# Optimization experiments

Measured on AMD Instinct MI355X. Metric: run time of the kernel, lower is better.

The kernel has to match this reference:

```python
import jax, jax.numpy as jnp
import numpy as np

N = 50000      # nodes
E = 800000     # edges (avg degree 16)
IN = 128       # in_dim0
H = 96         # hidden_dim
BN_EPS = 1e-5
PN_SCALE = 20.0


def setup_inputs() -> dict:
    key = jax.random.key(0)
    ks = jax.random.split(key, 12)
    s_in = 1.0 / np.sqrt(IN)
    s_h = 1.0 / np.sqrt(H)
    return {
        "x": jax.random.normal(ks[0], (N, IN), jnp.float32),
        "edge_index": jax.random.randint(ks[1], (2, E), 0, N, jnp.int32),
        # mlp0: Linear(in_dim0 -> hidden)
        "W0": jax.random.uniform(ks[2], (H, IN), jnp.float32, -s_in, s_in),
        "b0": jax.random.uniform(ks[3], (H,), jnp.float32, -s_in, s_in),
        # GIN MLP layer 1: Linear(hidden -> hidden) + BatchNorm
        "W1": jax.random.uniform(ks[4], (H, H), jnp.float32, -s_h, s_h),
        "b1": jax.random.uniform(ks[5], (H,), jnp.float32, -s_h, s_h),
        "gamma": jnp.ones((H,), jnp.float32),
        "beta": jnp.zeros((H,), jnp.float32),
        # GIN MLP layer 2: Linear(hidden -> hidden)
        "W2": jax.random.uniform(ks[6], (H, H), jnp.float32, -s_h, s_h),
        "b2": jax.random.uniform(ks[7], (H,), jnp.float32, -s_h, s_h),
    }


def reference(x, edge_index, W0, b0, W1, b1, gamma, beta, W2, b2):
    # h0 = mlp0(x)
    h0 = x @ W0.T + b0                                   # [N, H]

    # GINConv (eps=0): z_i = h0_i + sum_{j->i} h0_j
    src, dst = edge_index[0], edge_index[1]
    agg = jax.ops.segment_sum(h0[src], dst, num_segments=N)  # [N, H]
    z = h0 + agg

    # GIN MLP (layer_num=2): Linear -> BatchNorm(train) -> ReLU -> Linear
    h = z @ W1.T + b1
    mean = h.mean(axis=0)
    var = h.var(axis=0)                                  # biased, like torch BN
    h = (h - mean) * jax.lax.rsqrt(var + BN_EPS) * gamma + beta
    h = jax.nn.relu(h)
    l1 = h @ W2.T + b2                                   # [N, H]

    # PairNorm 'PN-SCS', scale=20
    col_mean = l1.mean(axis=0)
    rownorm = jnp.sqrt(1e-6 + jnp.sum(l1 * l1, axis=1, keepdims=True))
    l1 = PN_SCALE * l1 / rownorm - col_mean

    return (l1, h0)
```

## Files before the change

### kernel.cpp

```cpp
#include <hip/hip_runtime.h>

#define NN 50000
#define IN_DIM 128
#define HD 96
#define BN_EPS 1e-5f
#define PN_SCALE 20.0f
#define SCAN_NB 196
#define NREP 4

using bf16x8 = __attribute__((ext_vector_type(8))) short;
using f32x4  = __attribute__((ext_vector_type(4))) float;

__device__ __forceinline__ float4 ld4(const float* p) { return *(const float4*)p; }
__device__ __forceinline__ float4 add4(float4 a, float4 b) {
    return make_float4(a.x + b.x, a.y + b.y, a.z + b.z, a.w + b.w);
}

__device__ __forceinline__ short bfr(float f) {
    unsigned u = __float_as_uint(f);
    unsigned r = u + 0x7fffu + ((u >> 16) & 1u);
    return (short)(r >> 16);
}
__device__ __forceinline__ bf16x8 cvt8(float4 a, float4 b) {
    bf16x8 r;
    r[0] = bfr(a.x); r[1] = bfr(a.y); r[2] = bfr(a.z); r[3] = bfr(a.w);
    r[4] = bfr(b.x); r[5] = bfr(b.y); r[6] = bfr(b.z); r[7] = bfr(b.w);
    return r;
}

__global__ void zero_kernel(float* stats, int* cnt) {
    int i = blockIdx.x * blockDim.x + threadIdx.x;
    if (i < 1024) stats[i] = 0.0f;
    int j = i - 1024;
    if (j >= 0 && j < NREP * NN) cnt[j] = 0;
}

template<int K, int MODE>
__global__ __launch_bounds__(256) void gemm_mfma(
    const float* A, const float* __restrict__ W, const float* __restrict__ bias,
    float* out, const float* __restrict__ scale, const float* __restrict__ shift,
    float* __restrict__ gsum, float* __restrict__ gsumsq,
    float* __restrict__ gcol, float* __restrict__ growss,
    const int* __restrict__ ei, int* __restrict__ hist_cnt, int E)
{
    constexpr int P     = K + 8;
    constexpr int NS    = K / 32;
    constexpr int KD4   = K / 4;
    constexpr int WITER = (96 * KD4) / 256;
    constexpr int WL_SH  = 96 * P;
    constexpr int WL_TOT = (20608 > WL_SH) ? 20608 : WL_SH;
    __shared__ short Wl[WL_TOT];

    const int t    = threadIdx.x;
    const int l    = t & 63;
    const int w    = t >> 6;
    const int l15  = l & 15;
    const int lh   = l >> 4;
    const int base = blockIdx.x * 64;

    const int  arow = base + w * 16 + l15;
    const bool aok  = arow < NN;
    const float* Ap = A + (size_t)arow * K + lh * 8;
    const float4 Z4 = make_float4(0.f, 0.f, 0.f, 0.f);

    float4 pa[2 * NS];
#pragma unroll
    for (int s = 0; s < NS; ++s) {
        pa[2 * s]     = aok ? ld4(Ap + s * 32)     : Z4;
        pa[2 * s + 1] = aok ? ld4(Ap + s * 32 + 4) : Z4;
    }
    float4 wv[WITER];
#pragma unroll
    for (int i = 0; i < WITER; ++i) {
        int c = t + i * 256;
        int row = c / KD4, kq = c - row * KD4;
        wv[i] = ld4(W + (size_t)row * K + kq * 4);
    }
    float4 scv[2 * NS], shv[2 * NS];
    if (MODE == 2) {
#pragma unroll
        for (int s = 0; s < 2 * NS; ++s) {
            scv[s] = ld4(scale + (s >> 1) * 32 + lh * 8 + (s & 1) * 4);
            shv[s] = ld4(shift + (s >> 1) * 32 + lh * 8 + (s & 1) * 4);
        }
    }

    if (MODE == 0) {
        int e0 = (blockIdx.x * 256 + t) * 4;
        if (e0 + 4 <= E) {
            int4 d4 = *(const int4*)(ei + E + e0);
            atomicAdd(&hist_cnt[0 * NN + d4.x], 1);
            atomicAdd(&hist_cnt[1 * NN + d4.y], 1);
            atomicAdd(&hist_cnt[2 * NN + d4.z], 1);
            atomicAdd(&hist_cnt[3 * NN + d4.w], 1);
        } else {
            for (int i = 0; i < 4; ++i) {
                int e = e0 + i;
                if (e < E) atomicAdd(&hist_cnt[(e & 3) * NN + ei[E + e]], 1);
            }
        }
    }

    bf16x8 af[NS];
#pragma unroll
    for (int s = 0; s < NS; ++s) {
        float4 q0 = pa[2 * s], q1 = pa[2 * s + 1];
        if (MODE == 2) {
            float4 sc0 = scv[2 * s], sh0 = shv[2 * s];
            float4 sc1 = scv[2 * s + 1], sh1 = shv[2 * s + 1];
            q0.x = fmaxf(q0.x * sc0.x + sh0.x, 0.f);
            q0.y = fmaxf(q0.y * sc0.y + sh0.y, 0.f);
            q0.z = fmaxf(q0.z * sc0.z + sh0.z, 0.f);
            q0.w = fmaxf(q0.w * sc0.w + sh0.w, 0.f);
            q1.x = fmaxf(q1.x * sc1.x + sh1.x, 0.f);
            q1.y = fmaxf(q1.y * sc1.y + sh1.y, 0.f);
            q1.z = fmaxf(q1.z * sc1.z + sh1.z, 0.f);
            q1.w = fmaxf(q1.w * sc1.w + sh1.w, 0.f);
        }
        af[s] = cvt8(q0, q1);
    }

#pragma unroll
    for (int i = 0; i < WITER; ++i) {
        int c = t + i * 256;
        int row = c / KD4, kq = c - row * KD4;
        short4 s4v;
        s4v.x = bfr(wv[i].x); s4v.y = bfr(wv[i].y);
        s4v.z = bfr(wv[i].z); s4v.w = bfr(wv[i].w);
        *(short4*)(Wl + row * P + kq * 4) = s4v;
    }
    __syncthreads();

    f32x4 acc[6];
#pragma unroll
    for (int n = 0; n < 6; ++n) acc[n] = (f32x4){0.f, 0.f, 0.f, 0.f};

#pragma unroll
    for (int s = 0; s < NS; ++s) {
        const short* wp = Wl + s * 32 + lh * 8;
#pragma unroll
        for (int n = 0; n < 6; ++n) {
            bf16x8 bf = *(const bf16x8*)(wp + (n * 16 + l15) * P);
            acc[n] = __builtin_amdgcn_mfma_f32_16x16x32_bf16(af[s], bf, acc[n], 0, 0, 0);
        }
    }

    float cv[6][4];
#pragma unroll
    for (int n = 0; n < 6; ++n) {
        float b = bias[n * 16 + l15];
#pragma unroll
        for (int r = 0; r < 4; ++r) cv[n][r] = acc[n][r] + b;
    }
    int crow[4]; bool cok[4];
#pragma unroll
    for (int r = 0; r < 4; ++r) {
        crow[r] = base + w * 16 + lh * 4 + r;
        cok[r]  = crow[r] < NN;
    }

    __syncthreads();
    float* Cl = (float*)Wl;
#pragma unroll
    for (int n = 0; n < 6; ++n)
#pragma unroll
        for (int r = 0; r < 4; ++r)
            Cl[(w * 16 + lh * 4 + r) * 100 + n * 16 + l15] = cv[n][r];
    __syncthreads();
    {
        int lrow = t >> 2;
        int q4   = t & 3;
        int grow = base + lrow;
        if (grow < NN) {
            float* o = out + (size_t)grow * HD;
            const float* cr = Cl + lrow * 100;
#pragma unroll
            for (int k = 0; k < 6; ++k) {
                int c4 = q4 + k * 4;
                *(float4*)(o + c4 * 4) = *(const float4*)(cr + c4 * 4);
            }
        }
    }

    if (MODE == 1) {
        float s[6], q[6];
#pragma unroll
        for (int n = 0; n < 6; ++n) {
            s[n] = 0.f; q[n] = 0.f;
#pragma unroll
            for (int r = 0; r < 4; ++r) {
                float v = cok[r] ? cv[n][r] : 0.f;
                s[n] += v; q[n] += v * v;
            }
        }
#pragma unroll
        for (int n = 0; n < 6; ++n) {
            s[n] += __shfl_xor(s[n], 16); s[n] += __shfl_xor(s[n], 32);
            q[n] += __shfl_xor(q[n], 16); q[n] += __shfl_xor(q[n], 32);
        }
        float* red0 = (float*)Wl + 6400;
        float* red1 = red0 + 384;
        if (lh == 0) {
#pragma unroll
            for (int n = 0; n < 6; ++n) {
                red0[w * 96 + n * 16 + l15] = s[n];
                red1[w * 96 + n * 16 + l15] = q[n];
            }
        }
        __syncthreads();
        if (t < HD) {
            float S = red0[t] + red0[96 + t] + red0[192 + t] + red0[288 + t];
            float Q = red1[t] + red1[96 + t] + red1[192 + t] + red1[288 + t];
            atomicAdd(&gsum[t], S);
            atomicAdd(&gsumsq[t], Q);
        }
    }

    if (MODE == 2) {
        float s[6];
#pragma unroll
        for (int n = 0; n < 6; ++n) {
            s[n] = 0.f;
#pragma unroll
            for (int r = 0; r < 4; ++r) s[n] += cok[r] ? cv[n][r] : 0.f;
        }
#pragma unroll
        for (int n = 0; n < 6; ++n) {
            s[n] += __shfl_xor(s[n], 16); s[n] += __shfl_xor(s[n], 32);
        }
        float rq[4];
#pragma unroll
        for (int r = 0; r < 4; ++r) {
            float v = 0.f;
#pragma unroll
            for (int n = 0; n < 6; ++n) v = fmaf(cv[n][r], cv[n][r], v);
            v += __shfl_xor(v, 1); v += __shfl_xor(v, 2);
            v += __shfl_xor(v, 4); v += __shfl_xor(v, 8);
            rq[r] = v;
        }
        float* red0 = (float*)Wl + 6400;
        if (lh == 0) {
#pragma unroll
            for (int n = 0; n < 6; ++n) red0[w * 96 + n * 16 + l15] = s[n];
        }
        __syncthreads();
        if (t < HD) {
            float S = red0[t] + red0[96 + t] + red0[192 + t] + red0[288 + t];
            atomicAdd(&gcol[t], S);
        }
        if (l15 == 0) {
#pragma unroll
            for (int r = 0; r < 4; ++r)
                if (cok[r]) growss[crow[r]] = rq[r];
        }
    }
}

__global__ __launch_bounds__(256) void scan_part1(const int* __restrict__ cnt,
                                                  int* __restrict__ bsum) {
    __shared__ int sh[256];
    int i = blockIdx.x * 256 + threadIdx.x;
    int t = threadIdx.x;
    int v = 0;
    if (i < NN)
        v = cnt[i] + cnt[NN + i] + cnt[2 * NN + i] + cnt[3 * NN + i];
    sh[t] = v;
    __syncthreads();
    for (int off = 128; off > 0; off >>= 1) {
        if (t < off) sh[t] += sh[t + off];
        __syncthreads();
    }
    if (t == 0) bsum[blockIdx.x] = sh[0];
}

__global__ __launch_bounds__(256) void scan_part2(int* __restrict__ bsum) {
    __shared__ int sh[256];
    int t = threadIdx.x;
    int v = (t < SCAN_NB) ? bsum[t] : 0;
    sh[t] = v;
    __syncthreads();
    for (int off = 1; off < 256; off <<= 1) {
        int u = sh[t];
        if (t >= off) u += sh[t - off];
        __syncthreads();
        sh[t] = u;
        __syncthreads();
    }
    if (t < SCAN_NB) bsum[t] = sh[t] - v;
}

__global__ __launch_bounds__(256) void scan_part3(int* __restrict__ cnt,
                                                  const int* __restrict__ bsum,
                                                  int* __restrict__ rowptr) {
    __shared__ int sh[256];
    int i = blockIdx.x * 256 + threadIdx.x;
    int t = threadIdx.x;
    int v = 0;
    if (i < NN)
        v = cnt[i] + cnt[NN + i] + cnt[2 * NN + i] + cnt[3 * NN + i];
    sh[t] = v;
    __syncthreads();
    for (int off = 1; off < 256; off <<= 1) {
        int u = sh[t];
        if (t >= off) u += sh[t - off];
        __syncthreads();
        sh[t] = u;
        __syncthreads();
    }
    int excl = sh[t] - v + bsum[blockIdx.x];
    if (i < NN) { rowptr[i] = excl; cnt[i] = excl; }
    if (i == NN - 1) rowptr[NN] = excl + v;
}

__global__ __launch_bounds__(256) void fill_kernel(const int* __restrict__ ei,
                                                   int* __restrict__ cursor,
                                                   int* __restrict__ srcs, int E) {
    int t2 = blockIdx.x * 256 + threadIdx.x;
    int e0 = t2 * 2;
    int src[2], dst[2];
#pragma unroll
    for (int i = 0; i < 2; ++i) {
        int e = e0 + i;
        bool ok = e < E;
        dst[i] = ok ? ei[E + e] : -1;
        src[i] = ok ? ei[e] : 0;
    }
    for (int pass = 0; pass < 7; ++pass) {
#pragma unroll
        for (int i = 0; i < 2; ++i) {
            if (dst[i] >= 0 && (dst[i] >> 13) == pass) {
                int slot = atomicAdd(&cursor[dst[i]], 1);
                srcs[slot] = src[i];
            }
        }
    }
}

__global__ __launch_bounds__(192) void gather_kernel(
    const float* __restrict__ h0, const int* __restrict__ rowptr,
    const int* __restrict__ srcs, float* __restrict__ z)
{
    const int tid = threadIdx.x;
    const int rl  = tid / 24;
    const int c   = tid - rl * 24;
    const int row = blockIdx.x * 8 + rl;
    if (row >= NN) return;

    const int p0 = rowptr[row];
    const int p1 = rowptr[row + 1];

    float4 acc = ld4(h0 + (size_t)row * HD + c * 4);

    int p = p0;
    for (; p + 8 <= p1; p += 8) {
        int s0 = srcs[p + 0], s1 = srcs[p + 1], s2 = srcs[p + 2], s3 = srcs[p + 3];
        int s4 = srcs[p + 4], s5 = srcs[p + 5], s6 = srcs[p + 6], s7 = srcs[p + 7];
        float4 v0 = ld4(h0 + (size_t)s0 * HD + c * 4);
        float4 v1 = ld4(h0 + (size_t)s1 * HD + c * 4);
        float4 v2 = ld4(h0 + (size_t)s2 * HD + c * 4);
        float4 v3 = ld4(h0 + (size_t)s3 * HD + c * 4);
        float4 v4 = ld4(h0 + (size_t)s4 * HD + c * 4);
        float4 v5 = ld4(h0 + (size_t)s5 * HD + c * 4);
        float4 v6 = ld4(h0 + (size_t)s6 * HD + c * 4);
        float4 v7 = ld4(h0 + (size_t)s7 * HD + c * 4);
        acc = add4(acc, add4(add4(add4(v0, v1), add4(v2, v3)),
                             add4(add4(v4, v5), add4(v6, v7))));
    }
    for (; p + 4 <= p1; p += 4) {
        int s0 = srcs[p + 0], s1 = srcs[p + 1], s2 = srcs[p + 2], s3 = srcs[p + 3];
        float4 v0 = ld4(h0 + (size_t)s0 * HD + c * 4);
        float4 v1 = ld4(h0 + (size_t)s1 * HD + c * 4);
        float4 v2 = ld4(h0 + (size_t)s2 * HD + c * 4);
        float4 v3 = ld4(h0 + (size_t)s3 * HD + c * 4);
        acc = add4(acc, add4(add4(v0, v1), add4(v2, v3)));
    }
    for (; p < p1; ++p)
        acc = add4(acc, ld4(h0 + (size_t)srcs[p] * HD + c * 4));

    *(float4*)(z + (size_t)row * HD + c * 4) = acc;
}

__global__ void bn_finalize_kernel(const float* __restrict__ sum, const float* __restrict__ sumsq,
                                   const float* __restrict__ gamma, const float* __restrict__ beta,
                                   float* __restrict__ scale, float* __restrict__ shift)
{
    int f = threadIdx.x;
    if (f < HD) {
        float mean = sum[f] * (1.0f / NN);
        float var  = fmaxf(sumsq[f] * (1.0f / NN) - mean * mean, 0.0f);
        float rstd = rsqrtf(var + BN_EPS);
        float sc = rstd * gamma[f];
        scale[f] = sc;
        shift[f] = beta[f] - mean * sc;
    }
}

__global__ __launch_bounds__(256) void pn_kernel(float* l1, const float* __restrict__ colsum,
                                                 const float* __restrict__ rowss)
{
    int idx = blockIdx.x * 256 + threadIdx.x;
    if (idx >= NN * 24) return;
    int row = idx / 24;
    int q = idx - row * 24;
    float rs = rsqrtf(1e-6f + rowss[row]);
    float4 v = ld4(l1 + (size_t)idx * 4);
    float4 cm = ld4(colsum + q * 4);
    v.x = PN_SCALE * v.x * rs - cm.x * (1.0f / NN);
    v.y = PN_SCALE * v.y * rs - cm.y * (1.0f / NN);
    v.z = PN_SCALE * v.z * rs - cm.z * (1.0f / NN);
    v.w = PN_SCALE * v.w * rs - cm.w * (1.0f / NN);
    *(float4*)(l1 + (size_t)idx * 4) = v;
}

extern "C" void kernel_launch(void* const* d_in, const int* in_sizes, int n_in,
                              void* d_out, int out_size, void* d_ws, size_t ws_size,
                              hipStream_t stream) {
    const float* x     = (const float*)d_in[0];
    const int*   ei    = (const int*)d_in[1];
    const float* W0    = (const float*)d_in[2];
    const float* b0    = (const float*)d_in[3];
    const float* W1    = (const float*)d_in[4];
    const float* b1    = (const float*)d_in[5];
    const float* gamma = (const float*)d_in[6];
    const float* beta  = (const float*)d_in[7];
    const float* W2    = (const float*)d_in[8];
    const float* b2    = (const float*)d_in[9];

    float* out_l1 = (float*)d_out;
    float* out_h0 = out_l1 + (size_t)NN * HD;

    float* stats   = (float*)d_ws;
    float* s_sum   = stats;
    float* s_sumsq = stats + HD;
    float* s_col   = stats + 2 * HD;
    float* s_scale = stats + 288;
    float* s_shift = stats + 384;
    float* rowss = stats + 1024;
    int* cnt    = (int*)(rowss + NN);
    int* rowptr = cnt + NREP * NN;
    int* bsum   = rowptr + NN + 2;
    int* srcs   = bsum + 256;

    const int E = in_sizes[1] / 2;
    const int GB = (NN + 63) / 64;

    zero_kernel<<<(1024 + NREP * NN + 255) / 256, 256, 0, stream>>>(stats, cnt);
    gemm_mfma<IN_DIM, 0><<<GB, 256, 0, stream>>>(x, W0, b0, out_h0, nullptr, nullptr,
                                                 nullptr, nullptr, nullptr, nullptr,
                                                 ei, cnt, E);
    scan_part1<<<SCAN_NB, 256, 0, stream>>>(cnt, bsum);
    scan_part2<<<1, 256, 0, stream>>>(bsum);
    scan_part3<<<SCAN_NB, 256, 0, stream>>>(cnt, bsum, rowptr);
    fill_kernel<<<(E / 2 + 255) / 256, 256, 0, stream>>>(ei, cnt, srcs, E);
    gather_kernel<<<(NN + 7) / 8, 192, 0, stream>>>(out_h0, rowptr, srcs, out_l1);
    gemm_mfma<HD, 1><<<GB, 256, 0, stream>>>(out_l1, W1, b1, out_l1, nullptr, nullptr,
                                             s_sum, s_sumsq, nullptr, nullptr,
                                             nullptr, nullptr, 0);
    bn_finalize_kernel<<<1, 128, 0, stream>>>(s_sum, s_sumsq, gamma, beta, s_scale, s_shift);
    gemm_mfma<HD, 2><<<GB, 256, 0, stream>>>(out_l1, W2, b2, out_l1, s_scale, s_shift,
                                             nullptr, nullptr, s_col, rowss,
                                             nullptr, nullptr, 0);
    pn_kernel<<<(NN * 24 + 255) / 256, 256, 0, stream>>>(out_l1, s_col, rowss);
}
```

Baseline: 293.8 us.

## Gather neighbor features from a bf16 copy of h0 and store GEMM outputs directly

```diff
diff --git a/kernel.cpp b/kernel.cpp
--- a/kernel.cpp
+++ b/kernel.cpp
@@ -21,6 +21,9 @@
     unsigned r = u + 0x7fffu + ((u >> 16) & 1u);
     return (short)(r >> 16);
 }
+__device__ __forceinline__ float bf2f(unsigned short s) {
+    return __uint_as_float((unsigned)s << 16);
+}
 __device__ __forceinline__ bf16x8 cvt8(float4 a, float4 b) {
     bf16x8 r;
     r[0] = bfr(a.x); r[1] = bfr(a.y); r[2] = bfr(a.z); r[3] = bfr(a.w);
@@ -38,7 +41,8 @@
 template<int K, int MODE>
 __global__ __launch_bounds__(256) void gemm_mfma(
     const float* A, const float* __restrict__ W, const float* __restrict__ bias,
-    float* out, const float* __restrict__ scale, const float* __restrict__ shift,
+    float* out, unsigned short* __restrict__ out_bf,
+    const float* __restrict__ scale, const float* __restrict__ shift,
     float* __restrict__ gsum, float* __restrict__ gsumsq,
     float* __restrict__ gcol, float* __restrict__ growss,
     const int* __restrict__ ei, int* __restrict__ hist_cnt, int E)
@@ -159,25 +163,42 @@
         cok[r]  = crow[r] < NN;
     }
 
-    __syncthreads();
-    float* Cl = (float*)Wl;
-#pragma unroll
-    for (int n = 0; n < 6; ++n)
-#pragma unroll
-        for (int r = 0; r < 4; ++r)
-            Cl[(w * 16 + lh * 4 + r) * 100 + n * 16 + l15] = cv[n][r];
-    __syncthreads();
-    {
+    if (MODE == 0) {
+        __syncthreads();
+        float* Cl = (float*)Wl;
+#pragma unroll
+        for (int n = 0; n < 6; ++n)
+#pragma unroll
+            for (int r = 0; r < 4; ++r)
+                Cl[(w * 16 + lh * 4 + r) * 100 + n * 16 + l15] = cv[n][r];
+        __syncthreads();
         int lrow = t >> 2;
         int q4   = t & 3;
         int grow = base + lrow;
         if (grow < NN) {
             float* o = out + (size_t)grow * HD;
+            unsigned short* ob = out_bf + (size_t)grow * HD;
             const float* cr = Cl + lrow * 100;
 #pragma unroll
             for (int k = 0; k < 6; ++k) {
                 int c4 = q4 + k * 4;
-                *(float4*)(o + c4 * 4) = *(const float4*)(cr + c4 * 4);
+                float4 v = *(const float4*)(cr + c4 * 4);
+                *(float4*)(o + c4 * 4) = v;
+                ushort4 sv;
+                sv.x = (unsigned short)bfr(v.x);
+                sv.y = (unsigned short)bfr(v.y);
+                sv.z = (unsigned short)bfr(v.z);
+                sv.w = (unsigned short)bfr(v.w);
+                *(ushort4*)(ob + c4 * 4) = sv;
+            }
+        }
+    } else {
+#pragma unroll
+        for (int r = 0; r < 4; ++r) {
+            if (cok[r]) {
+                float* o = out + (size_t)crow[r] * HD + l15;
+#pragma unroll
+                for (int n = 0; n < 6; ++n) o[n * 16] = cv[n][r];
             }
         }
     }
@@ -198,7 +219,8 @@
             s[n] += __shfl_xor(s[n], 16); s[n] += __shfl_xor(s[n], 32);
             q[n] += __shfl_xor(q[n], 16); q[n] += __shfl_xor(q[n], 32);
         }
-        float* red0 = (float*)Wl + 6400;
+        __syncthreads();
+        float* red0 = (float*)Wl;
         float* red1 = red0 + 384;
         if (lh == 0) {
 #pragma unroll
@@ -238,7 +260,8 @@
             v += __shfl_xor(v, 4); v += __shfl_xor(v, 8);
             rq[r] = v;
         }
-        float* red0 = (float*)Wl + 6400;
+        __syncthreads();
+        float* red0 = (float*)Wl;
         if (lh == 0) {
 #pragma unroll
             for (int n = 0; n < 6; ++n) red0[w * 96 + n * 16 + l15] = s[n];
@@ -337,8 +360,9 @@
 }
 
 __global__ __launch_bounds__(192) void gather_kernel(
-    const float* __restrict__ h0, const int* __restrict__ rowptr,
-    const int* __restrict__ srcs, float* __restrict__ z)
+    const float* __restrict__ h0, const unsigned short* __restrict__ h0b,
+    const int* __restrict__ rowptr, const int* __restrict__ srcs,
+    float* __restrict__ z)
 {
     const int tid = threadIdx.x;
     const int rl  = tid / 24;
@@ -355,27 +379,28 @@
     for (; p + 8 <= p1; p += 8) {
         int s0 = srcs[p + 0], s1 = srcs[p + 1], s2 = srcs[p + 2], s3 = srcs[p + 3];
         int s4 = srcs[p + 4], s5 = srcs[p + 5], s6 = srcs[p + 6], s7 = srcs[p + 7];
-        float4 v0 = ld4(h0 + (size_t)s0 * HD + c * 4);
-        float4 v1 = ld4(h0 + (size_t)s1 * HD + c * 4);
-        float4 v2 = ld4(h0 + (size_t)s2 * HD + c * 4);
-        float4 v3 = ld4(h0 + (size_t)s3 * HD + c * 4);
-        float4 v4 = ld4(h0 + (size_t)s4 * HD + c * 4);
-        float4 v5 = ld4(h0 + (size_t)s5 * HD + c * 4);
-        float4 v6 = ld4(h0 + (size_t)s6 * HD + c * 4);
-        float4 v7 = ld4(h0 + (size_t)s7 * HD + c * 4);
-        acc = add4(acc, add4(add4(add4(v0, v1), add4(v2, v3)),
-                             add4(add4(v4, v5), add4(v6, v7))));
-    }
-    for (; p + 4 <= p1; p += 4) {
-        int s0 = srcs[p + 0], s1 = srcs[p + 1], s2 = srcs[p + 2], s3 = srcs[p + 3];
-        float4 v0 = ld4(h0 + (size_t)s0 * HD + c * 4);
-        float4 v1 = ld4(h0 + (size_t)s1 * HD + c * 4);
-        float4 v2 = ld4(h0 + (size_t)s2 * HD + c * 4);
-        float4 v3 = ld4(h0 + (size_t)s3 * HD + c * 4);
-        acc = add4(acc, add4(add4(v0, v1), add4(v2, v3)));
-    }
-    for (; p < p1; ++p)
-        acc = add4(acc, ld4(h0 + (size_t)srcs[p] * HD + c * 4));
+        ushort4 v0 = *(const ushort4*)(h0b + (size_t)s0 * HD + c * 4);
+        ushort4 v1 = *(const ushort4*)(h0b + (size_t)s1 * HD + c * 4);
+        ushort4 v2 = *(const ushort4*)(h0b + (size_t)s2 * HD + c * 4);
+        ushort4 v3 = *(const ushort4*)(h0b + (size_t)s3 * HD + c * 4);
+        ushort4 v4 = *(const ushort4*)(h0b + (size_t)s4 * HD + c * 4);
+        ushort4 v5 = *(const ushort4*)(h0b + (size_t)s5 * HD + c * 4);
+        ushort4 v6 = *(const ushort4*)(h0b + (size_t)s6 * HD + c * 4);
+        ushort4 v7 = *(const ushort4*)(h0b + (size_t)s7 * HD + c * 4);
+        acc.x += bf2f(v0.x) + bf2f(v1.x) + bf2f(v2.x) + bf2f(v3.x)
+               + bf2f(v4.x) + bf2f(v5.x) + bf2f(v6.x) + bf2f(v7.x);
+        acc.y += bf2f(v0.y) + bf2f(v1.y) + bf2f(v2.y) + bf2f(v3.y)
+               + bf2f(v4.y) + bf2f(v5.y) + bf2f(v6.y) + bf2f(v7.y);
+        acc.z += bf2f(v0.z) + bf2f(v1.z) + bf2f(v2.z) + bf2f(v3.z)
+               + bf2f(v4.z) + bf2f(v5.z) + bf2f(v6.z) + bf2f(v7.z);
+        acc.w += bf2f(v0.w) + bf2f(v1.w) + bf2f(v2.w) + bf2f(v3.w)
+               + bf2f(v4.w) + bf2f(v5.w) + bf2f(v6.w) + bf2f(v7.w);
+    }
+    for (; p < p1; ++p) {
+        ushort4 v = *(const ushort4*)(h0b + (size_t)srcs[p] * HD + c * 4);
+        acc.x += bf2f(v.x); acc.y += bf2f(v.y);
+        acc.z += bf2f(v.z); acc.w += bf2f(v.w);
+    }
 
     *(float4*)(z + (size_t)row * HD + c * 4) = acc;
 }
@@ -440,24 +465,29 @@
     int* rowptr = cnt + NREP * NN;
     int* bsum   = rowptr + NN + 2;
     int* srcs   = bsum + 256;
+    unsigned short* h0b =
+        (unsigned short*)(((uintptr_t)(srcs + 800000) + 15) & ~(uintptr_t)15);
 
     const int E = in_sizes[1] / 2;
     const int GB = (NN + 63) / 64;
 
     zero_kernel<<<(1024 + NREP * NN + 255) / 256, 256, 0, stream>>>(stats, cnt);
-    gemm_mfma<IN_DIM, 0><<<GB, 256, 0, stream>>>(x, W0, b0, out_h0, nullptr, nullptr,
+    gemm_mfma<IN_DIM, 0><<<GB, 256, 0, stream>>>(x, W0, b0, out_h0, h0b,
+                                                 nullptr, nullptr,
                                                  nullptr, nullptr, nullptr, nullptr,
                                                  ei, cnt, E);
     scan_part1<<<SCAN_NB, 256, 0, stream>>>(cnt, bsum);
     scan_part2<<<1, 256, 0, stream>>>(bsum);
     scan_part3<<<SCAN_NB, 256, 0, stream>>>(cnt, bsum, rowptr);
     fill_kernel<<<(E / 2 + 255) / 256, 256, 0, stream>>>(ei, cnt, srcs, E);
-    gather_kernel<<<(NN + 7) / 8, 192, 0, stream>>>(out_h0, rowptr, srcs, out_l1);
-    gemm_mfma<HD, 1><<<GB, 256, 0, stream>>>(out_l1, W1, b1, out_l1, nullptr, nullptr,
+    gather_kernel<<<(NN + 7) / 8, 192, 0, stream>>>(out_h0, h0b, rowptr, srcs, out_l1);
+    gemm_mfma<HD, 1><<<GB, 256, 0, stream>>>(out_l1, W1, b1, out_l1, nullptr,
+                                             nullptr, nullptr,
                                              s_sum, s_sumsq, nullptr, nullptr,
                                              nullptr, nullptr, 0);
     bn_finalize_kernel<<<1, 128, 0, stream>>>(s_sum, s_sumsq, gamma, beta, s_scale, s_shift);
-    gemm_mfma<HD, 2><<<GB, 256, 0, stream>>>(out_l1, W2, b2, out_l1, s_scale, s_shift,
+    gemm_mfma<HD, 2><<<GB, 256, 0, stream>>>(out_l1, W2, b2, out_l1, nullptr,
+                                             s_scale, s_shift,
                                              nullptr, nullptr, s_col, rowss,
                                              nullptr, nullptr, 0);
     pn_kernel<<<(NN * 24 + 255) / 256, 256, 0, stream>>>(out_l1, s_col, rowss);
```

After: 287.0 us. -2.3%, faster.
